# Kernel tuning notes

Measured on AMD Instinct MI355X. Metric: run time of the kernel, lower is better.

## Reference

```python
import jax, jax.numpy as jnp
import numpy as np

N_NODES = 100000
N_EDGES = 1600000
IN_DIM, HID_DIM, OUT_DIM = 128, 256, 64


def setup_inputs() -> dict:
    key = jax.random.key(0)
    ks = jax.random.split(key, 8)
    h = jax.random.normal(ks[0], (N_NODES, IN_DIM), dtype=jnp.float32)
    W1 = jax.random.normal(ks[1], (IN_DIM, HID_DIM), dtype=jnp.float32) * (1.0 / np.sqrt(IN_DIM))
    b1 = jnp.zeros((HID_DIM,), dtype=jnp.float32)
    W2 = jax.random.normal(ks[2], (HID_DIM, OUT_DIM), dtype=jnp.float32) * (1.0 / np.sqrt(HID_DIM))
    b2 = jnp.zeros((OUT_DIM,), dtype=jnp.float32)
    p = jax.random.uniform(ks[3], (HID_DIM,), dtype=jnp.float32)  # variational dropout retain probs
    src = jax.random.randint(ks[4], (N_EDGES,), 0, N_NODES, dtype=jnp.int32)
    dst = jax.random.randint(ks[5], (N_EDGES,), 0, N_NODES, dtype=jnp.int32)
    return {"h": h, "W1": W1, "b1": b1, "W2": W2, "b2": b2, "p": p,
            "src": src, "dst": dst, "n_nodes": N_NODES}


def _gcn_norms(src, dst, n_nodes, dtype):
    # DGL GraphConv norm='both': D_out^{-1/2} on source side, D_in^{-1/2} on dest side,
    # degrees clamped to min 1.
    ones = jnp.ones(src.shape, dtype=dtype)
    deg_out = jnp.clip(jax.ops.segment_sum(ones, src, num_segments=n_nodes), 1.0, None)
    deg_in = jnp.clip(jax.ops.segment_sum(ones, dst, num_segments=n_nodes), 1.0, None)
    return deg_out ** -0.5, deg_in ** -0.5


def _spmm(x, src, dst, n_nodes):
    # sum-aggregate src features into dst nodes (copy_u + sum)
    return jax.ops.segment_sum(x[src], dst, num_segments=n_nodes)


def reference(h, W1, b1, W2, b2, p, src, dst, n_nodes):
    norm_src, norm_dst = _gcn_norms(src, dst, n_nodes, h.dtype)

    # --- GraphConv 1 (in 128 <= out 256: aggregate first, then weight) ---
    x = h * norm_src[:, None]
    x = _spmm(x, src, dst, n_nodes)              # [N, IN_DIM]
    x = x * norm_dst[:, None]
    x = x @ W1 + b1                               # [N, HID_DIM]
    x = jax.nn.relu(x)

    # --- deterministic variational dropout: scale by clamp(p, 0, 1) ---
    x = x * jnp.clip(p, 0.0, 1.0)[None, :]

    # --- GraphConv 2 (in 256 > out 64: weight first, then aggregate) ---
    y = x @ W2                                    # [N, OUT_DIM]
    y = y * norm_src[:, None]
    y = _spmm(y, src, dst, n_nodes)
    y = y * norm_dst[:, None] + b2
    return y
```

## Files before the change

kernel.cpp:

```cpp
#include <hip/hip_runtime.h>

#define IN_DIM 128
#define HID 256
#define OUTD 64
#define NB 256

typedef __attribute__((ext_vector_type(8))) short bf16x8;
typedef __attribute__((ext_vector_type(4))) float f32x4;
typedef __attribute__((ext_vector_type(8))) unsigned short ushort8v;

__device__ __forceinline__ unsigned short f2bf(float x) {
    unsigned int u = __float_as_uint(x);
    unsigned int r = (u + 0x7fffu + ((u >> 16) & 1u)) >> 16;
    return (unsigned short)r;
}
__device__ __forceinline__ float bf2f(unsigned short b) {
    return __uint_as_float(((unsigned int)b) << 16);
}


__global__ __launch_bounds__(256) void k_bucketA(const int* __restrict__ src,
                                                 const int* __restrict__ dst,
                                                 int* __restrict__ partS, int* __restrict__ partD,
                                                 int E, int NBK) {
    __shared__ int hS[512], hD[512];
    int b = blockIdx.x, t = threadIdx.x;
    for (int j = t; j < 512; j += 256) { hS[j] = 0; hD[j] = 0; }
    __syncthreads();
    int chunk = (E + NB - 1) / NB;
    int e0 = b * chunk, e1 = min(E, e0 + chunk);
    for (int e = e0 + t; e < e1; e += 256) {
        atomicAdd(&hS[src[e] >> 8], 1);
        atomicAdd(&hD[dst[e] >> 8], 1);
    }
    __syncthreads();
    for (int j = t; j < NBK; j += 256) {
        partS[j * NB + b] = hS[j];
        partD[j * NB + b] = hD[j];
    }
}

__global__ __launch_bounds__(256) void k_bscanP(int* __restrict__ partS, int* __restrict__ partD,
                                                int* __restrict__ totS, int* __restrict__ totD) {
    __shared__ int sS[256], sD[256];
    int j = blockIdx.x, t = threadIdx.x;
    int vS = partS[j * NB + t], vD = partD[j * NB + t];
    sS[t] = vS; sD[t] = vD;
    __syncthreads();
    for (int o = 1; o < 256; o <<= 1) {
        int xS = (t >= o) ? sS[t - o] : 0;
        int xD = (t >= o) ? sD[t - o] : 0;
        __syncthreads();
        sS[t] += xS; sD[t] += xD;
        __syncthreads();
    }
    partS[j * NB + t] = sS[t] - vS;
    partD[j * NB + t] = sD[t] - vD;
    if (t == 255) { totS[j] = sS[255]; totD[j] = sD[255]; }
}

__global__ __launch_bounds__(512) void k_bscanT(const int* __restrict__ totS,
                                                const int* __restrict__ totD,
                                                int* __restrict__ sOff, int* __restrict__ dOff,
                                                int* __restrict__ eoff,
                                                int N, int E, int NBK) {
    __shared__ int sS[512], sD[512];
    int t = threadIdx.x;
    int vS = (t < NBK) ? totS[t] : 0;
    int vD = (t < NBK) ? totD[t] : 0;
    sS[t] = vS; sD[t] = vD;
    __syncthreads();
    for (int o = 1; o < 512; o <<= 1) {
        int xS = (t >= o) ? sS[t - o] : 0;
        int xD = (t >= o) ? sD[t - o] : 0;
        __syncthreads();
        sS[t] += xS; sD[t] += xD;
        __syncthreads();
    }
    if (t < NBK) { sOff[t] = sS[t] - vS; dOff[t] = sD[t] - vD; }
    if (t == 0) { sOff[NBK] = E; dOff[NBK] = E; eoff[N] = E; }
}

__global__ __launch_bounds__(256) void k_bucketB2(const int* __restrict__ src,
                                                  const int* __restrict__ dst,
                                                  const int* __restrict__ partS,
                                                  const int* __restrict__ partD,
                                                  const int* __restrict__ sOff,
                                                  const int* __restrict__ dOff,
                                                  unsigned int* __restrict__ dpairs,
                                                  unsigned char* __restrict__ sloc,
                                                  int E, int NBK) {
    __shared__ int cS[512], cD[512];
    int b = blockIdx.x, t = threadIdx.x;
    for (int j = t; j < NBK; j += 256) {
        cS[j] = partS[j * NB + b] + sOff[j];
        cD[j] = partD[j * NB + b] + dOff[j];
    }
    __syncthreads();
    int chunk = (E + NB - 1) / NB;
    int e0 = b * chunk, e1 = min(E, e0 + chunk);
    for (int e = e0 + t; e < e1; e += 256) {
        int s = src[e], d = dst[e];
        int pD = atomicAdd(&cD[d >> 8], 1);
        dpairs[pD] = ((unsigned int)(d & 255) << 17) | (unsigned int)s;
        int pS = atomicAdd(&cS[s >> 8], 1);
        sloc[pS] = (unsigned char)(s & 255);
    }
}

__global__ __launch_bounds__(256) void k_bucketC(const unsigned int* __restrict__ dpairs,
                                                 const int* __restrict__ dOff,
                                                 int* __restrict__ eoff,
                                                 int* __restrict__ esrc,
                                                 float* __restrict__ nd,
                                                 int N) {
    __shared__ int hist[256], sc[256], cur[256];
    int b = blockIdx.x, t = threadIdx.x;
    int base = dOff[b], end = dOff[b + 1];
    hist[t] = 0;
    __syncthreads();
    for (int i = base + t; i < end; i += 256)
        atomicAdd(&hist[dpairs[i] >> 17], 1);
    __syncthreads();
    int cnt = hist[t];
    int v = b * 256 + t;
    if (v < N) nd[v] = rsqrtf((float)max(cnt, 1));
    sc[t] = cnt;
    __syncthreads();
    for (int o = 1; o < 256; o <<= 1) {
        int x = (t >= o) ? sc[t - o] : 0;
        __syncthreads();
        sc[t] += x;
        __syncthreads();
    }
    int excl = sc[t] - cnt;
    if (v < N) eoff[v] = base + excl;
    cur[t] = excl;
    __syncthreads();
    for (int i = base + t; i < end; i += 256) {
        unsigned int pk = dpairs[i];
        int pos = atomicAdd(&cur[pk >> 17], 1);
        esrc[base + pos] = (int)(pk & 0x1FFFFu);
    }
}

__global__ __launch_bounds__(256) void k_bucketCs(const unsigned char* __restrict__ sloc,
                                                  const int* __restrict__ sOff,
                                                  float* __restrict__ ns,
                                                  int N) {
    __shared__ int hist[256];
    int b = blockIdx.x, t = threadIdx.x;
    int base = sOff[b], end = sOff[b + 1];
    hist[t] = 0;
    __syncthreads();
    for (int i = base + t; i < end; i += 256)
        atomicAdd(&hist[sloc[i]], 1);
    __syncthreads();
    int v = b * 256 + t;
    if (v < N) ns[v] = rsqrtf((float)max(hist[t], 1));
}

__global__ void k_hconv(const float* __restrict__ h, const float* __restrict__ ns,
                        unsigned short* __restrict__ hb, int total4) {
    int i = blockIdx.x * 256 + threadIdx.x;
    if (i >= total4) return;
    int node = i >> 5;
    float nsv = ns[node];
    float4 v = ((const float4*)h)[i];
    ushort4 o;
    o.x = f2bf(v.x * nsv);
    o.y = f2bf(v.y * nsv);
    o.z = f2bf(v.z * nsv);
    o.w = f2bf(v.w * nsv);
    ((ushort4*)hb)[i] = o;
}

__global__ void k_wprep(const float* __restrict__ W1, const float* __restrict__ W2,
                        unsigned short* __restrict__ Wt1, unsigned short* __restrict__ Wt2) {
    int t = blockIdx.x * 256 + threadIdx.x;
    if (t < IN_DIM * HID) {
        int k = t & (IN_DIM - 1), n = t >> 7;
        Wt1[(size_t)n * IN_DIM + k] = f2bf(W1[(size_t)k * HID + n]);
    }
    if (t < HID * OUTD) {
        int k = t & (HID - 1), n = t >> 8;
        Wt2[(size_t)n * HID + k] = f2bf(W2[(size_t)k * OUTD + n]);
    }
}

__global__ __launch_bounds__(256) void k_spmm1(const unsigned short* __restrict__ hb,
                                               const int* __restrict__ eoff,
                                               const int* __restrict__ esrc,
                                               const float* __restrict__ nd,
                                               unsigned short* __restrict__ xb, int N) {
    int wid = threadIdx.x >> 6;
    int v = blockIdx.x * 4 + wid;
    if (v >= N) return;
    int l = threadIdx.x & 63;
    int c = l & 15, el = l >> 4;
    int s0 = eoff[v], s1 = eoff[v + 1];

    float a0[8] = {0.f, 0.f, 0.f, 0.f, 0.f, 0.f, 0.f, 0.f};
    float a1[8] = {0.f, 0.f, 0.f, 0.f, 0.f, 0.f, 0.f, 0.f};
    int i = s0 + el;
    for (; i + 4 < s1; i += 8) {
        int sA = esrc[i], sB = esrc[i + 4];
        ushort8v uA = *(const ushort8v*)(hb + (size_t)sA * IN_DIM + c * 8);
        ushort8v uB = *(const ushort8v*)(hb + (size_t)sB * IN_DIM + c * 8);
#pragma unroll
        for (int k = 0; k < 8; ++k) {
            a0[k] += bf2f((unsigned short)uA[k]);
            a1[k] += bf2f((unsigned short)uB[k]);
        }
    }
    for (; i < s1; i += 4) {
        int sA = esrc[i];
        ushort8v uA = *(const ushort8v*)(hb + (size_t)sA * IN_DIM + c * 8);
#pragma unroll
        for (int k = 0; k < 8; ++k) a0[k] += bf2f((unsigned short)uA[k]);
    }
    float s[8];
#pragma unroll
    for (int k = 0; k < 8; ++k) {
        float x = a0[k] + a1[k];
        x += __shfl_xor(x, 16);
        x += __shfl_xor(x, 32);
        s[k] = x;
    }
    if (el == 0) {
        float ndv = nd[v];
        uint4 o;
        unsigned int* op = (unsigned int*)&o;
#pragma unroll
        for (int k = 0; k < 4; ++k) {
            unsigned int lo = f2bf(s[2 * k] * ndv);
            unsigned int hi = f2bf(s[2 * k + 1] * ndv);
            op[k] = lo | (hi << 16);
        }
        *(uint4*)(xb + (size_t)v * IN_DIM + c * 8) = o;
    }
}

template <int EPI>
__global__ __launch_bounds__(256) void k_mgemm(const unsigned short* __restrict__ A,
                                               const unsigned short* __restrict__ Bt,
                                               const float* __restrict__ b1,
                                               const float* __restrict__ p,
                                               const float* __restrict__ ns,
                                               unsigned short* __restrict__ outp,
                                               int M) {
    constexpr int BM = (EPI == 1) ? 64 : 256;
    constexpr int BN = (EPI == 1) ? 256 : 64;
    constexpr int K = (EPI == 1) ? 128 : 256;
    constexpr int OUT_LD = (EPI == 1) ? 256 : 64;
    __shared__ unsigned short As[BM * 64];
    __shared__ unsigned short Bs[BN * 64];
    const int t = threadIdx.x, w = t >> 6, l = t & 63;
    const int row0 = blockIdx.x * BM;
    const int wm0 = (EPI == 1) ? 0 : w * 64;
    const int wn0 = (EPI == 1) ? w * 64 : 0;
    const int lr = l & 15, lk = (l >> 4) * 8, lg = l >> 4;

    f32x4 acc[4][4] = {};

    for (int k0 = 0; k0 < K; k0 += 64) {
#pragma unroll
        for (int q = 0; q < BM / 32; ++q) {
            int chunk = w * (BM / 32) + q;
            int gr = row0 + chunk * 8 + (l >> 3);
            if (gr > M - 1) gr = M - 1;
            const unsigned short* gp = A + (size_t)gr * K + k0 + (l & 7) * 8;
            __builtin_amdgcn_global_load_lds((const __attribute__((address_space(1))) void*)gp,
                                             (__attribute__((address_space(3))) void*)&As[chunk * 512], 16, 0, 0);
        }
#pragma unroll
        for (int q = 0; q < BN / 32; ++q) {
            int chunk = w * (BN / 32) + q;
            int r = chunk * 8 + (l >> 3);
            const unsigned short* gp = Bt + (size_t)r * K + k0 + (l & 7) * 8;
            __builtin_amdgcn_global_load_lds((const __attribute__((address_space(1))) void*)gp,
                                             (__attribute__((address_space(3))) void*)&Bs[chunk * 512], 16, 0, 0);
        }
        __syncthreads();

#pragma unroll
        for (int kk = 0; kk < 2; ++kk) {
            bf16x8 a[4], b[4];
#pragma unroll
            for (int m = 0; m < 4; ++m)
                a[m] = *(const bf16x8*)&As[(wm0 + m * 16 + lr) * 64 + kk * 32 + lk];
#pragma unroll
            for (int n = 0; n < 4; ++n)
                b[n] = *(const bf16x8*)&Bs[(wn0 + n * 16 + lr) * 64 + kk * 32 + lk];
#pragma unroll
            for (int m = 0; m < 4; ++m)
#pragma unroll
                for (int n = 0; n < 4; ++n)
                    acc[m][n] = __builtin_amdgcn_mfma_f32_16x16x32_bf16(a[m], b[n], acc[m][n], 0, 0, 0);
        }
        __syncthreads();
    }

#pragma unroll
    for (int n = 0; n < 4; ++n) {
        int col = wn0 + n * 16 + lr;
        float bb = 0.f, pp = 1.f;
        if (EPI == 1) {
            bb = b1[col];
            pp = fminf(fmaxf(p[col], 0.f), 1.f);
        }
#pragma unroll
        for (int m = 0; m < 4; ++m) {
#pragma unroll
            for (int j = 0; j < 4; ++j) {
                int row = row0 + wm0 + m * 16 + lg * 4 + j;
                if (row < M) {
                    float v = acc[m][n][j];
                    if (EPI == 1) {
                        v = fmaxf(v + bb, 0.f) * pp;
                    } else {
                        v *= ns[row];
                    }
                    outp[(size_t)row * OUT_LD + col] = f2bf(v);
                }
            }
        }
    }
}

__global__ __launch_bounds__(256) void k_spmm2(const unsigned short* __restrict__ ybf,
                                               const int* __restrict__ eoff,
                                               const int* __restrict__ esrc,
                                               const float* __restrict__ nd,
                                               const float* __restrict__ b2,
                                               float* __restrict__ out, int N) {
    int wid = threadIdx.x >> 6;
    int v = blockIdx.x * 4 + wid;
    if (v >= N) return;
    int l = threadIdx.x & 63;
    int c = l & 15, el = l >> 4;
    int s0 = eoff[v], s1 = eoff[v + 1];

    float ax0 = 0.f, ay0 = 0.f, az0 = 0.f, aw0 = 0.f;
    float ax1 = 0.f, ay1 = 0.f, az1 = 0.f, aw1 = 0.f;
    int i = s0 + el;
    for (; i + 4 < s1; i += 8) {
        int sA = esrc[i], sB = esrc[i + 4];
        ushort4 uA = *(const ushort4*)(ybf + (size_t)sA * OUTD + c * 4);
        ushort4 uB = *(const ushort4*)(ybf + (size_t)sB * OUTD + c * 4);
        ax0 += bf2f(uA.x); ay0 += bf2f(uA.y); az0 += bf2f(uA.z); aw0 += bf2f(uA.w);
        ax1 += bf2f(uB.x); ay1 += bf2f(uB.y); az1 += bf2f(uB.z); aw1 += bf2f(uB.w);
    }
    for (; i < s1; i += 4) {
        ushort4 u = *(const ushort4*)(ybf + (size_t)esrc[i] * OUTD + c * 4);
        ax0 += bf2f(u.x); ay0 += bf2f(u.y); az0 += bf2f(u.z); aw0 += bf2f(u.w);
    }
    float ax = ax0 + ax1, ay = ay0 + ay1, az = az0 + az1, aw = aw0 + aw1;
    ax += __shfl_xor(ax, 16); ax += __shfl_xor(ax, 32);
    ay += __shfl_xor(ay, 16); ay += __shfl_xor(ay, 32);
    az += __shfl_xor(az, 16); az += __shfl_xor(az, 32);
    aw += __shfl_xor(aw, 16); aw += __shfl_xor(aw, 32);
    if (l < 16) {
        float ndv = nd[v];
        float4 bb = *(const float4*)(b2 + c * 4);
        float4 o;
        o.x = ax * ndv + bb.x;
        o.y = ay * ndv + bb.y;
        o.z = az * ndv + bb.z;
        o.w = aw * ndv + bb.w;
        *(float4*)(out + (size_t)v * OUTD + c * 4) = o;
    }
}

extern "C" void kernel_launch(void* const* d_in, const int* in_sizes, int n_in,
                              void* d_out, int out_size, void* d_ws, size_t ws_size,
                              hipStream_t stream) {
    const float* h  = (const float*)d_in[0];
    const float* W1 = (const float*)d_in[1];
    const float* b1 = (const float*)d_in[2];
    const float* W2 = (const float*)d_in[3];
    const float* b2 = (const float*)d_in[4];
    const float* p  = (const float*)d_in[5];
    const int* src  = (const int*)d_in[6];
    const int* dst  = (const int*)d_in[7];

    const int N = in_sizes[0] / IN_DIM;
    const int E = in_sizes[6];
    const int NBK = (N + 255) >> 8;
    float* out = (float*)d_out;

    char* ws = (char*)d_ws;
    size_t off = 0;
    auto alloc = [&](size_t bytes) -> void* {
        void* ptr = ws + off;
        off = (off + bytes + 255) & ~(size_t)255;
        return ptr;
    };
    int* sOff = (int*)alloc(513 * 4);
    int* dOff = (int*)alloc(513 * 4);
    int* totS = (int*)alloc(512 * 4);
    int* totD = (int*)alloc(512 * 4);
    int* eoff = (int*)alloc((size_t)(N + 1) * 4);
    int* esrc = (int*)alloc((size_t)E * 4);
    float* ns = (float*)alloc((size_t)N * 4);
    float* nd = (float*)alloc((size_t)N * 4);
    unsigned short* hb  = (unsigned short*)alloc((size_t)N * IN_DIM * 2);
    unsigned short* xb  = (unsigned short*)alloc((size_t)N * IN_DIM * 2);
    unsigned short* hid = (unsigned short*)alloc((size_t)N * HID * 2);
    unsigned short* Wt1 = (unsigned short*)alloc((size_t)HID * IN_DIM * 2);
    unsigned short* Wt2 = (unsigned short*)alloc((size_t)OUTD * HID * 2);
    unsigned short* ybf = xb;
    unsigned int* dpairs = (unsigned int*)hid;
    unsigned char* sloc  = (unsigned char*)hid + (size_t)E * 4;
    int* partS = (int*)((char*)hid + ((size_t)E * 5 + 255 & ~(size_t)255));
    int* partD = partS + 512 * NB;

    int tpb = 256;
    k_bucketA<<<NB, 256, 0, stream>>>(src, dst, partS, partD, E, NBK);
    k_bscanP<<<NBK, 256, 0, stream>>>(partS, partD, totS, totD);
    k_bscanT<<<1, 512, 0, stream>>>(totS, totD, sOff, dOff, eoff, N, E, NBK);
    k_bucketB2<<<NB, 256, 0, stream>>>(src, dst, partS, partD, sOff, dOff, dpairs, sloc, E, NBK);
    k_bucketC<<<NBK, 256, 0, stream>>>(dpairs, dOff, eoff, esrc, nd, N);
    k_bucketCs<<<NBK, 256, 0, stream>>>(sloc, sOff, ns, N);

    int total4 = N * (IN_DIM / 4);
    k_hconv<<<(total4 + tpb - 1) / tpb, tpb, 0, stream>>>(h, ns, hb, total4);

    k_wprep<<<(IN_DIM * HID + 255) / 256, 256, 0, stream>>>(W1, W2, Wt1, Wt2);

    k_spmm1<<<(N + 3) / 4, 256, 0, stream>>>(hb, eoff, esrc, nd, xb, N);

    k_mgemm<1><<<(N + 63) / 64, 256, 0, stream>>>(xb, Wt1, b1, p, nullptr, hid, N);

    k_mgemm<2><<<(N + 255) / 256, 256, 0, stream>>>(hid, Wt2, nullptr, nullptr, ns, ybf, N);

    k_spmm2<<<(N + 3) / 4, 256, 0, stream>>>(ybf, eoff, esrc, nd, b2, out, N);
}
```

Before: 348.9 us.

## Fuse weight prep and h conversion into bucket kernels; widen SpMM edge unrolling

The W1/W2 transpose-and-convert step moves into k_bucketA, and the bf16 conversion of h is merged into the source-degree kernel, now named k_nsconv, which computes ns in shared memory and scales its own 256-node block. Together these drop two kernel launches and one reload of ns. Both SpMM kernels now process four gathered edges per iteration instead of two, unpacking bf16 pairs into float2 vectors so more loads are in flight and the adds are packed. The trade-off is that the h conversion now runs on only one block per 256 nodes, each doing more work, which lowers parallelism for that step, and the wider unroll uses more registers.

```diff
diff --git a/kernel.cpp b/kernel.cpp
--- a/kernel.cpp
+++ b/kernel.cpp
@@ -7,7 +7,7 @@
 
 typedef __attribute__((ext_vector_type(8))) short bf16x8;
 typedef __attribute__((ext_vector_type(4))) float f32x4;
-typedef __attribute__((ext_vector_type(8))) unsigned short ushort8v;
+typedef __attribute__((ext_vector_type(2))) float f32x2;
 
 __device__ __forceinline__ unsigned short f2bf(float x) {
     unsigned int u = __float_as_uint(x);
@@ -17,14 +17,32 @@
 __device__ __forceinline__ float bf2f(unsigned short b) {
     return __uint_as_float(((unsigned int)b) << 16);
 }
+__device__ __forceinline__ f32x2 up2(unsigned int u) {
+    f32x2 r;
+    r.x = __uint_as_float(u << 16);
+    r.y = __uint_as_float(u & 0xffff0000u);
+    return r;
+}
 
 
 __global__ __launch_bounds__(256) void k_bucketA(const int* __restrict__ src,
                                                  const int* __restrict__ dst,
                                                  int* __restrict__ partS, int* __restrict__ partD,
+                                                 const float* __restrict__ W1, const float* __restrict__ W2,
+                                                 unsigned short* __restrict__ Wt1,
+                                                 unsigned short* __restrict__ Wt2,
                                                  int E, int NBK) {
     __shared__ int hS[512], hD[512];
     int b = blockIdx.x, t = threadIdx.x;
+    int g = b * 256 + t;
+    if (g < IN_DIM * HID) {
+        int k = g & (IN_DIM - 1), n = g >> 7;
+        Wt1[(size_t)n * IN_DIM + k] = f2bf(W1[(size_t)k * HID + n]);
+    }
+    if (g < HID * OUTD) {
+        int k = g & (HID - 1), n = g >> 8;
+        Wt2[(size_t)n * HID + k] = f2bf(W2[(size_t)k * OUTD + n]);
+    }
     for (int j = t; j < 512; j += 256) { hS[j] = 0; hD[j] = 0; }
     __syncthreads();
     int chunk = (E + NB - 1) / NB;
@@ -144,11 +162,14 @@
     }
 }
 
-__global__ __launch_bounds__(256) void k_bucketCs(const unsigned char* __restrict__ sloc,
-                                                  const int* __restrict__ sOff,
-                                                  float* __restrict__ ns,
-                                                  int N) {
+__global__ __launch_bounds__(256) void k_nsconv(const unsigned char* __restrict__ sloc,
+                                                const int* __restrict__ sOff,
+                                                const float* __restrict__ h,
+                                                float* __restrict__ ns,
+                                                unsigned short* __restrict__ hb,
+                                                int N) {
     __shared__ int hist[256];
+    __shared__ float nsf[256];
     int b = blockIdx.x, t = threadIdx.x;
     int base = sOff[b], end = sOff[b + 1];
     hist[t] = 0;
@@ -157,34 +178,23 @@
         atomicAdd(&hist[sloc[i]], 1);
     __syncthreads();
     int v = b * 256 + t;
-    if (v < N) ns[v] = rsqrtf((float)max(hist[t], 1));
-}
-
-__global__ void k_hconv(const float* __restrict__ h, const float* __restrict__ ns,
-                        unsigned short* __restrict__ hb, int total4) {
-    int i = blockIdx.x * 256 + threadIdx.x;
-    if (i >= total4) return;
-    int node = i >> 5;
-    float nsv = ns[node];
-    float4 v = ((const float4*)h)[i];
-    ushort4 o;
-    o.x = f2bf(v.x * nsv);
-    o.y = f2bf(v.y * nsv);
-    o.z = f2bf(v.z * nsv);
-    o.w = f2bf(v.w * nsv);
-    ((ushort4*)hb)[i] = o;
-}
-
-__global__ void k_wprep(const float* __restrict__ W1, const float* __restrict__ W2,
-                        unsigned short* __restrict__ Wt1, unsigned short* __restrict__ Wt2) {
-    int t = blockIdx.x * 256 + threadIdx.x;
-    if (t < IN_DIM * HID) {
-        int k = t & (IN_DIM - 1), n = t >> 7;
-        Wt1[(size_t)n * IN_DIM + k] = f2bf(W1[(size_t)k * HID + n]);
-    }
-    if (t < HID * OUTD) {
-        int k = t & (HID - 1), n = t >> 8;
-        Wt2[(size_t)n * HID + k] = f2bf(W2[(size_t)k * OUTD + n]);
+    float nsv = rsqrtf((float)max(hist[t], 1));
+    nsf[t] = nsv;
+    if (v < N) ns[v] = nsv;
+    __syncthreads();
+    int vb = b * 256;
+    for (int idx = t; idx < 256 * 32; idx += 256) {
+        int row = idx >> 5, col = idx & 31;
+        if (vb + row < N) {
+            float nv = nsf[row];
+            float4 x = ((const float4*)h)[(size_t)(vb + row) * 32 + col];
+            ushort4 o;
+            o.x = f2bf(x.x * nv);
+            o.y = f2bf(x.y * nv);
+            o.z = f2bf(x.z * nv);
+            o.w = f2bf(x.w * nv);
+            ((ushort4*)hb)[(size_t)(vb + row) * 32 + col] = o;
+        }
     }
 }
 
@@ -200,32 +210,32 @@
     int c = l & 15, el = l >> 4;
     int s0 = eoff[v], s1 = eoff[v + 1];
 
-    float a0[8] = {0.f, 0.f, 0.f, 0.f, 0.f, 0.f, 0.f, 0.f};
-    float a1[8] = {0.f, 0.f, 0.f, 0.f, 0.f, 0.f, 0.f, 0.f};
+    f32x2 a0[4] = {}, a1[4] = {}, a2[4] = {}, a3[4] = {};
     int i = s0 + el;
-    for (; i + 4 < s1; i += 8) {
-        int sA = esrc[i], sB = esrc[i + 4];
-        ushort8v uA = *(const ushort8v*)(hb + (size_t)sA * IN_DIM + c * 8);
-        ushort8v uB = *(const ushort8v*)(hb + (size_t)sB * IN_DIM + c * 8);
-#pragma unroll
-        for (int k = 0; k < 8; ++k) {
-            a0[k] += bf2f((unsigned short)uA[k]);
-            a1[k] += bf2f((unsigned short)uB[k]);
-        }
+    for (; i + 12 < s1; i += 16) {
+        int sA = esrc[i], sB = esrc[i + 4], sC = esrc[i + 8], sD = esrc[i + 12];
+        uint4 uA = *(const uint4*)(hb + (size_t)sA * IN_DIM + c * 8);
+        uint4 uB = *(const uint4*)(hb + (size_t)sB * IN_DIM + c * 8);
+        uint4 uC = *(const uint4*)(hb + (size_t)sC * IN_DIM + c * 8);
+        uint4 uD = *(const uint4*)(hb + (size_t)sD * IN_DIM + c * 8);
+        a0[0] += up2(uA.x); a0[1] += up2(uA.y); a0[2] += up2(uA.z); a0[3] += up2(uA.w);
+        a1[0] += up2(uB.x); a1[1] += up2(uB.y); a1[2] += up2(uB.z); a1[3] += up2(uB.w);
+        a2[0] += up2(uC.x); a2[1] += up2(uC.y); a2[2] += up2(uC.z); a2[3] += up2(uC.w);
+        a3[0] += up2(uD.x); a3[1] += up2(uD.y); a3[2] += up2(uD.z); a3[3] += up2(uD.w);
     }
     for (; i < s1; i += 4) {
         int sA = esrc[i];
-        ushort8v uA = *(const ushort8v*)(hb + (size_t)sA * IN_DIM + c * 8);
-#pragma unroll
-        for (int k = 0; k < 8; ++k) a0[k] += bf2f((unsigned short)uA[k]);
+        uint4 uA = *(const uint4*)(hb + (size_t)sA * IN_DIM + c * 8);
+        a0[0] += up2(uA.x); a0[1] += up2(uA.y); a0[2] += up2(uA.z); a0[3] += up2(uA.w);
     }
     float s[8];
 #pragma unroll
-    for (int k = 0; k < 8; ++k) {
-        float x = a0[k] + a1[k];
-        x += __shfl_xor(x, 16);
-        x += __shfl_xor(x, 32);
-        s[k] = x;
+    for (int j = 0; j < 4; ++j) {
+        f32x2 tj = (a0[j] + a1[j]) + (a2[j] + a3[j]);
+        float x0 = tj.x, x1 = tj.y;
+        x0 += __shfl_xor(x0, 16); x0 += __shfl_xor(x0, 32);
+        x1 += __shfl_xor(x1, 16); x1 += __shfl_xor(x1, 32);
+        s[2 * j] = x0; s[2 * j + 1] = x1;
     }
     if (el == 0) {
         float ndv = nd[v];
@@ -341,21 +351,26 @@
     int c = l & 15, el = l >> 4;
     int s0 = eoff[v], s1 = eoff[v + 1];
 
-    float ax0 = 0.f, ay0 = 0.f, az0 = 0.f, aw0 = 0.f;
-    float ax1 = 0.f, ay1 = 0.f, az1 = 0.f, aw1 = 0.f;
+    f32x2 q0[2] = {}, q1[2] = {}, q2[2] = {}, q3[2] = {};
     int i = s0 + el;
-    for (; i + 4 < s1; i += 8) {
-        int sA = esrc[i], sB = esrc[i + 4];
-        ushort4 uA = *(const ushort4*)(ybf + (size_t)sA * OUTD + c * 4);
-        ushort4 uB = *(const ushort4*)(ybf + (size_t)sB * OUTD + c * 4);
-        ax0 += bf2f(uA.x); ay0 += bf2f(uA.y); az0 += bf2f(uA.z); aw0 += bf2f(uA.w);
-        ax1 += bf2f(uB.x); ay1 += bf2f(uB.y); az1 += bf2f(uB.z); aw1 += bf2f(uB.w);
+    for (; i + 12 < s1; i += 16) {
+        int sA = esrc[i], sB = esrc[i + 4], sC = esrc[i + 8], sD = esrc[i + 12];
+        uint2 uA = *(const uint2*)(ybf + (size_t)sA * OUTD + c * 4);
+        uint2 uB = *(const uint2*)(ybf + (size_t)sB * OUTD + c * 4);
+        uint2 uC = *(const uint2*)(ybf + (size_t)sC * OUTD + c * 4);
+        uint2 uD = *(const uint2*)(ybf + (size_t)sD * OUTD + c * 4);
+        q0[0] += up2(uA.x); q0[1] += up2(uA.y);
+        q1[0] += up2(uB.x); q1[1] += up2(uB.y);
+        q2[0] += up2(uC.x); q2[1] += up2(uC.y);
+        q3[0] += up2(uD.x); q3[1] += up2(uD.y);
     }
     for (; i < s1; i += 4) {
-        ushort4 u = *(const ushort4*)(ybf + (size_t)esrc[i] * OUTD + c * 4);
-        ax0 += bf2f(u.x); ay0 += bf2f(u.y); az0 += bf2f(u.z); aw0 += bf2f(u.w);
-    }
-    float ax = ax0 + ax1, ay = ay0 + ay1, az = az0 + az1, aw = aw0 + aw1;
+        uint2 u = *(const uint2*)(ybf + (size_t)esrc[i] * OUTD + c * 4);
+        q0[0] += up2(u.x); q0[1] += up2(u.y);
+    }
+    f32x2 t0 = (q0[0] + q1[0]) + (q2[0] + q3[0]);
+    f32x2 t1 = (q0[1] + q1[1]) + (q2[1] + q3[1]);
+    float ax = t0.x, ay = t0.y, az = t1.x, aw = t1.y;
     ax += __shfl_xor(ax, 16); ax += __shfl_xor(ax, 32);
     ay += __shfl_xor(ay, 16); ay += __shfl_xor(ay, 32);
     az += __shfl_xor(az, 16); az += __shfl_xor(az, 32);
@@ -415,18 +430,12 @@
     int* partS = (int*)((char*)hid + ((size_t)E * 5 + 255 & ~(size_t)255));
     int* partD = partS + 512 * NB;
 
-    int tpb = 256;
-    k_bucketA<<<NB, 256, 0, stream>>>(src, dst, partS, partD, E, NBK);
+    k_bucketA<<<NB, 256, 0, stream>>>(src, dst, partS, partD, W1, W2, Wt1, Wt2, E, NBK);
     k_bscanP<<<NBK, 256, 0, stream>>>(partS, partD, totS, totD);
     k_bscanT<<<1, 512, 0, stream>>>(totS, totD, sOff, dOff, eoff, N, E, NBK);
     k_bucketB2<<<NB, 256, 0, stream>>>(src, dst, partS, partD, sOff, dOff, dpairs, sloc, E, NBK);
     k_bucketC<<<NBK, 256, 0, stream>>>(dpairs, dOff, eoff, esrc, nd, N);
-    k_bucketCs<<<NBK, 256, 0, stream>>>(sloc, sOff, ns, N);
-
-    int total4 = N * (IN_DIM / 4);
-    k_hconv<<<(total4 + tpb - 1) / tpb, tpb, 0, stream>>>(h, ns, hb, total4);
-
-    k_wprep<<<(IN_DIM * HID + 255) / 256, 256, 0, stream>>>(W1, W2, Wt1, Wt2);
+    k_nsconv<<<NBK, 256, 0, stream>>>(sloc, sOff, h, ns, hb, N);
 
     k_spmm1<<<(N + 3) / 4, 256, 0, stream>>>(hb, eoff, esrc, nd, xb, N);
 
```

New measurement: 382.9 us. +9.8%, slower.
